# Kernel tuning notes

Hardware: AMD Instinct MI355X
Metric: run time of the kernel (lower is better)

The kernel has to match this reference:

```python
import jax, jax.numpy as jnp
import numpy as np

N_ELEMENTS = 64  # StructureElementLayer(n_elements=64)


def setup_inputs() -> dict:
    key = jax.random.key(0)
    k1, k2 = jax.random.split(key)
    # x: [N, C, T, V] skeleton sequence (batch, coord channels, time, joints)
    x = jax.random.normal(k1, (256, 3, 256, 25), dtype=jnp.float32)
    # StructureElementLayer parameters (torch.rand init / ones*3 init)
    centres = jax.random.uniform(k2, (N_ELEMENTS, 2), dtype=jnp.float32)
    sharpness = jnp.ones((N_ELEMENTS, 2), dtype=jnp.float32) * 3.0
    return {"x": x, "centres": centres, "sharpness": sharpness}


def _mst_deaths(D):
    """Dim-0 Vietoris-Rips persistence deaths == MST edge weights (Prim's algorithm).

    D: [n, n] symmetric distance matrix. Returns [n-1] finite death values
    (births are all 0; the single essential (0, inf) pair contributes
    exp(-inf)=0 to the structure-element layer and is dropped).
    """
    n = D.shape[0]
    in_tree = jnp.zeros((n,), dtype=bool).at[0].set(True)
    dist = D[0]  # min distance from each node to the current tree

    def step(carry, _):
        in_tree, dist = carry
        d = jnp.where(in_tree, jnp.inf, dist)
        j = jnp.argmin(d)
        w = d[j]
        in_tree = in_tree.at[j].set(True)
        dist = jnp.minimum(dist, D[j])
        return (in_tree, dist), w

    (_, _), deaths = jax.lax.scan(step, (in_tree, dist), None, length=n - 1)
    return deaths


def _forward(x, centres, sharpness):
    xm = x.mean(1)                                  # [N, T, V]
    diff = xm[..., :, None] - xm[..., None, :]      # [N, T, V, V] pairwise joint diffs
    diff = diff.mean(-3)                            # [N, V, V]
    feat = jnp.linalg.norm(diff, axis=1)            # [N, V]  (torch.norm(., 2, dim=1))
    feat = (feat - feat.min()) / (feat.max() - feat.min())
    # Euclidean distance matrix of the N points in V-dim space (grad-safe sqrt)
    sq = jnp.sum(feat * feat, axis=1)
    D2 = sq[:, None] + sq[None, :] - 2.0 * (feat @ feat.T)
    D2 = jnp.maximum(D2, 0.0)
    D = jnp.where(D2 > 0.0, jnp.sqrt(jnp.where(D2 > 0.0, D2, 1.0)), 0.0)
    deaths = _mst_deaths(D)                         # [N-1]
    diag = jnp.stack([jnp.zeros_like(deaths), deaths], axis=-1)  # [N-1, 2] (birth, death)
    # StructureElementLayer: sum_i exp(-sum_d (p_id - c_kd)^2 * s_kd^2)
    d2 = (diag[:, None, :] - centres[None, :, :]) ** 2            # [N-1, K, 2]
    out = jnp.exp(-(d2 * (sharpness ** 2)).sum(-1)).sum(0)        # [K]
    return out


def reference(x, centres, sharpness):
    return _forward(x, centres, sharpness)
```

## Files before the change

### kernel.cpp

```cpp
#include <hip/hip_runtime.h>
#include <hip/hip_fp16.h>


#define WS_M    0
#define WS_MM   25600
#define WS_RK   28672
#define WS_D16  65536

#define INF32 0xFFFFFFFFu

__global__ void k_mean(const float* __restrict__ x, float* __restrict__ m) {
    const int n = blockIdx.x;
    const int tid = threadIdx.x;
    __shared__ float sums[25];
    if (tid < 25) sums[tid] = 0.0f;
    __syncthreads();
    if (tid < 200) {
        const float* base = x + (long)n * 19200 + 4 * tid;
        float a0 = 0.f, a1 = 0.f, a2 = 0.f, a3 = 0.f;
        #pragma unroll
        for (int i = 0; i < 24; ++i) {
            float4 v = *reinterpret_cast<const float4*>(base + 800 * i);
            a0 += v.x; a1 += v.y; a2 += v.z; a3 += v.w;
        }
        const int v0 = (4 * tid) % 25;
        atomicAdd(&sums[v0], a0);
        atomicAdd(&sums[(v0 + 1) % 25], a1);
        atomicAdd(&sums[(v0 + 2) % 25], a2);
        atomicAdd(&sums[(v0 + 3) % 25], a3);
    }
    __syncthreads();
    if (tid < 25) m[n * 25 + tid] = sums[tid] * (1.0f / 768.0f);
}

template <int CTRL>
__device__ __forceinline__ unsigned int dpp_min_step(unsigned int v) {
    unsigned int t = (unsigned int)__builtin_amdgcn_update_dpp(
        (int)0xFFFFFFFF, (int)v, CTRL, 0xF, 0xF, false);
    return (t < v) ? t : v;
}

__global__ void __launch_bounds__(256) k_dist(const float* __restrict__ m,
                                              unsigned short* __restrict__ D16,
                                              unsigned int* __restrict__ rowKeyG,
                                              unsigned int* __restrict__ mm) {
    __shared__ float mS[6400];
    __shared__ float featS[6400];
    __shared__ unsigned int bmin, bmax;
    __shared__ unsigned int wred[4];
    const int i = blockIdx.x;
    const int t = threadIdx.x;
    if (t == 0) { bmin = 0x7F800000u; bmax = 0u; }
    #pragma unroll
    for (int it = 0; it < 7; ++it) {
        int o = it * 256 + t;
        if (o < 1600) reinterpret_cast<float4*>(mS)[o] =
            reinterpret_cast<const float4*>(m)[o];
    }
    __syncthreads();
    float r[25];
    #pragma unroll
    for (int v = 0; v < 25; ++v) r[v] = mS[t * 25 + v];
    float S1 = 0.f, S2 = 0.f;
    #pragma unroll
    for (int v = 0; v < 25; ++v) { S1 += r[v]; S2 += r[v] * r[v]; }
    float fmn = 1e30f, fmx = -1e30f;
    #pragma unroll
    for (int w = 0; w < 25; ++w) {
        float q = S2 - 2.f * r[w] * S1 + 25.f * r[w] * r[w];
        q = fmaxf(q, 0.f);
        float f = sqrtf(q);
        featS[t * 25 + w] = f;
        fmn = fminf(fmn, f); fmx = fmaxf(fmx, f);
    }
    if (i == 0) {
        atomicMin(&bmin, __float_as_uint(fmn));
        atomicMax(&bmax, __float_as_uint(fmx));
    }
    __syncthreads();
    if (i == 0 && t == 0) { mm[0] = bmin; mm[1] = bmax; }
    float fi[25];
    #pragma unroll
    for (int v = 0; v < 25; ++v) fi[v] = featS[i * 25 + v];
    float s = 0.f;
    #pragma unroll
    for (int v = 0; v < 25; ++v) { float d = fi[v] - featS[t * 25 + v]; s += d * d; }
    const unsigned int w16 = (unsigned int)__half_as_ushort(__float2half(s));
    D16[i * 256 + t] = (unsigned short)w16;
    const unsigned int lo = (i < t) ? i : t, hi = (i < t) ? t : i;
    unsigned int key = (t == i) ? INF32 : ((w16 << 16) | (lo << 8) | hi);
    key = dpp_min_step<0x111>(key);
    key = dpp_min_step<0x112>(key);
    key = dpp_min_step<0x114>(key);
    key = dpp_min_step<0x118>(key);
    key = dpp_min_step<0x142>(key);
    key = dpp_min_step<0x143>(key);
    if ((t & 63) == 63) wred[t >> 6] = key;
    __syncthreads();
    if (t == 0) {
        unsigned int b0 = wred[0] < wred[1] ? wred[0] : wred[1];
        unsigned int b1 = wred[2] < wred[3] ? wred[2] : wred[3];
        rowKeyG[i] = b0 < b1 ? b0 : b1;
    }
}

#define SA 132
#define SB 68
#define OFF_B (128 * SA)

__device__ __forceinline__ void wave0_phase(int n, int lane,
        unsigned int* rowKeyS, unsigned char* parentS, unsigned char* newidS,
        unsigned char* cmapS, float* deaths, unsigned int* ncS, unsigned int* dcS) {
    unsigned int par[4];
    #pragma unroll
    for (int s = 0; s < 4; ++s) {
        const int i = lane + 64 * s;
        if (i < n) {
            const unsigned int rk = rowKeyS[i];
            const unsigned int u = (rk >> 8) & 0xFFu, v = rk & 0xFFu;
            unsigned int p = (u == (unsigned int)i) ? v : u;
            if (rk == INF32) p = (unsigned int)i;
            par[s] = p;
            parentS[i] = (unsigned char)p;
        }
    }
    #pragma unroll
    for (int s = 0; s < 4; ++s) {
        const int i = lane + 64 * s;
        if (i < n) {
            const unsigned int p = par[s];
            if (p != (unsigned int)i) {
                const unsigned int mp = parentS[p];
                if (mp == (unsigned int)i && (unsigned int)i < p) {
                    parentS[i] = (unsigned char)i;
                } else {
                    const unsigned int d = atomicAdd(dcS, 1u);
                    const unsigned int rk = rowKeyS[i];
                    deaths[d] = sqrtf(__half2float(__ushort_as_half(
                        (unsigned short)(rk >> 16))));
                }
            }
        }
    }
    for (;;) {
        bool ch = false;
        #pragma unroll
        for (int s = 0; s < 4; ++s) {
            const int i = lane + 64 * s;
            if (i < n) {
                const unsigned char p0 = parentS[i];
                const unsigned char np = parentS[p0];
                if (np != p0) { ch = true; parentS[i] = np; }
            }
        }
        if (__ballot(ch) == 0ull) break;
    }
    #pragma unroll
    for (int s = 0; s < 4; ++s) {
        const int i = lane + 64 * s;
        if (i < n && parentS[i] == (unsigned char)i)
            newidS[i] = (unsigned char)atomicAdd(ncS, 1u);
    }
    #pragma unroll
    for (int s = 0; s < 4; ++s) {
        const int i = lane + 64 * s;
        if (i < n) cmapS[i] = newidS[parentS[i]];
    }
}

__global__ void __launch_bounds__(1024) k_mst(const unsigned short* __restrict__ D16g,
                                              const unsigned int* __restrict__ rowKeyG,
                                              const unsigned int* __restrict__ mm,
                                              const float* __restrict__ centres,
                                              const float* __restrict__ sharp,
                                              float* __restrict__ out) {
    __shared__ unsigned int Mb[128 * SA + 64 * SB];
    __shared__ unsigned int rowKeyS[256];
    __shared__ unsigned char parentS[256], newidS[256];
    __shared__ __align__(8) unsigned char cmapS[256];
    __shared__ unsigned int ncS, dcS;
    __shared__ float deaths[256];
    __shared__ float outpart[1024];
    const int tid = threadIdx.x;

    if (tid < 256) rowKeyS[tid] = rowKeyG[tid];
    if (tid == 0) { ncS = 0; dcS = 0; }
    __syncthreads();
    if (tid < 64)
        wave0_phase(256, tid, rowKeyS, parentS, newidS, cmapS, deaths, &ncS, &dcS);
    __syncthreads();
    int n = (int)ncS;

    if (n > 1) {
        for (int w = tid; w < n * SA; w += 1024) Mb[w] = INF32;
        __syncthreads();
        const int r = tid & 255, q = tid >> 8, jb0 = q * 64;
        const unsigned int cr = cmapS[r];
        const uint4* src = reinterpret_cast<const uint4*>(D16g) + r * 32 + q * 8;
        const uint2* cmv = reinterpret_cast<const uint2*>(cmapS);
        #pragma unroll
        for (int c8 = 0; c8 < 8; ++c8) {
            const uint4 w4 = src[c8];
            const uint2 c2 = cmv[q * 8 + c8];
            const unsigned int wds[4] = {w4.x, w4.y, w4.z, w4.w};
            const unsigned int cbs[2] = {c2.x, c2.y};
            #pragma unroll
            for (int u = 0; u < 8; ++u) {
                const unsigned int cj = (cbs[u >> 2] >> (8 * (u & 3))) & 0xFFu;
                if (cj != cr) {
                    const unsigned int w16 = (wds[u >> 1] >> (16 * (u & 1))) & 0xFFFFu;
                    const unsigned int lo = cr < cj ? cr : cj;
                    const unsigned int hi = cr < cj ? cj : cr;
                    atomicMin(&Mb[cr * SA + cj], (w16 << 16) | (lo << 8) | hi);
                }
            }
        }
        __syncthreads();
    }

    int srcOff = 0, srcStr = SA, dstOff = OFF_B, dstStr = SB;
    while (n > 1) {
        if (tid < n) rowKeyS[tid] = INF32;
        if (tid == 0) ncS = 0;
        __syncthreads();
        if (tid < 8 * n) {
            const int a = tid >> 3, sub = tid & 7;
            const unsigned int* row = &Mb[srcOff + a * srcStr];
            unsigned int best = INF32;
            for (int b = sub; b < n; b += 8) {
                const unsigned int v = row[b];
                best = v < best ? v : best;
            }
            if (best != INF32) atomicMin(&rowKeyS[a], best);
        }
        __syncthreads();
        if (tid < 64)
            wave0_phase(n, tid, rowKeyS, parentS, newidS, cmapS, deaths, &ncS, &dcS);
        __syncthreads();
        const int nc = (int)ncS;
        if (nc > 1) {
            for (int w = tid; w < nc * dstStr; w += 1024) Mb[dstOff + w] = INF32;
            __syncthreads();
            if (tid < 8 * n) {
                const int a = tid >> 3, sub = tid & 7;
                const unsigned int ca = cmapS[a];
                const unsigned int* row = &Mb[srcOff + a * srcStr];
                for (int b = sub; b < n; b += 8) {
                    const unsigned int cb = cmapS[b];
                    const unsigned int v = row[b];
                    if (ca != cb && v != INF32) {
                        const unsigned int lo = ca < cb ? ca : cb;
                        const unsigned int hi = ca < cb ? cb : ca;
                        atomicMin(&Mb[dstOff + ca * dstStr + cb],
                                  (v & 0xFFFF0000u) | (lo << 8) | hi);
                    }
                }
            }
            __syncthreads();
        }
        const int t1 = srcOff; srcOff = dstOff; dstOff = t1;
        const int t2 = srcStr; srcStr = dstStr; dstStr = t2;
        n = nc;
    }

    const float mn = __uint_as_float(mm[0]);
    const float mx = __uint_as_float(mm[1]);
    const float inv = 1.0f / (mx - mn);
    const int k = tid & 63;
    const int part = tid >> 6;
    const float c0 = centres[2 * k], c1 = centres[2 * k + 1];
    const float s0 = sharp[2 * k],   s1 = sharp[2 * k + 1];
    const float t0 = c0 * c0 * s0 * s0;
    const float s1sq = s1 * s1;
    float acc = 0.f;
    for (int idx = part; idx < 255; idx += 16) {
        const float d = deaths[idx] * inv - c1;
        acc += __expf(-(t0 + d * d * s1sq));
    }
    outpart[tid] = acc;
    __syncthreads();
    if (tid < 64) {
        float s = 0.f;
        #pragma unroll
        for (int pp = 0; pp < 16; ++pp) s += outpart[tid + 64 * pp];
        out[tid] = s;
    }
}

extern "C" void kernel_launch(void* const* d_in, const int* in_sizes, int n_in,
                              void* d_out, int out_size, void* d_ws, size_t ws_size,
                              hipStream_t stream) {
    const float* x       = (const float*)d_in[0];
    const float* centres = (const float*)d_in[1];
    const float* sharp   = (const float*)d_in[2];
    float* out = (float*)d_out;
    char* ws = (char*)d_ws;
    float*          m   = (float*)(ws + WS_M);
    unsigned int*   mm  = (unsigned int*)(ws + WS_MM);
    unsigned int*   rk  = (unsigned int*)(ws + WS_RK);
    unsigned short* D16 = (unsigned short*)(ws + WS_D16);

    k_mean<<<256, 256, 0, stream>>>(x, m);
    k_dist<<<256, 256, 0, stream>>>(m, D16, rk, mm);
    k_mst<<<1, 1024, 0, stream>>>(D16, rk, mm, centres, sharp, out);
}
```

Baseline: 96.03 us.

## Offload first Boruvka contraction to a parallel multi-block kernel

Adds a new k_contract kernel with 256 blocks. Each block recomputes the first component labelling and scatters its row of the 16-bit distance matrix into a global contracted matrix with global atomicMin. The single-block k_mst then only copies that matrix into LDS instead of running 65536 atomic updates itself. The contracted matrix is initialised inside k_mean. Component renumbering now uses a wave ballot/popcount prefix instead of atomicAdd, and the round loop is capped at 12. The trade-off is an extra kernel launch, global atomics and redundant labelling work in every block.

```diff
diff --git a/kernel.cpp b/kernel.cpp
--- a/kernel.cpp
+++ b/kernel.cpp
@@ -6,12 +6,16 @@
 #define WS_MM   25600
 #define WS_RK   28672
 #define WS_D16  65536
+#define WS_MP   196608
 
 #define INF32 0xFFFFFFFFu
-
-__global__ void k_mean(const float* __restrict__ x, float* __restrict__ m) {
+#define MPSTR 132
+
+__global__ void k_mean(const float* __restrict__ x, float* __restrict__ m,
+                       unsigned int* __restrict__ Mp) {
     const int n = blockIdx.x;
     const int tid = threadIdx.x;
+    if (tid < 66) Mp[n * 66 + tid] = INF32;
     __shared__ float sums[25];
     if (tid < 25) sums[tid] = 0.0f;
     __syncthreads();
@@ -104,10 +108,7 @@
     }
 }
 
-#define SA 132
-#define SB 68
-#define OFF_B (128 * SA)
-
+template <bool RECORD>
 __device__ __forceinline__ void wave0_phase(int n, int lane,
         unsigned int* rowKeyS, unsigned char* parentS, unsigned char* newidS,
         unsigned char* cmapS, float* deaths, unsigned int* ncS, unsigned int* dcS) {
@@ -130,10 +131,9 @@
         if (i < n) {
             const unsigned int p = par[s];
             if (p != (unsigned int)i) {
-                const unsigned int mp = parentS[p];
-                if (mp == (unsigned int)i && (unsigned int)i < p) {
+                if (parentS[p] == (unsigned char)i && (unsigned int)i < p) {
                     parentS[i] = (unsigned char)i;
-                } else {
+                } else if (RECORD) {
                     const unsigned int d = atomicAdd(dcS, 1u);
                     const unsigned int rk = rowKeyS[i];
                     deaths[d] = sqrtf(__half2float(__ushort_as_half(
@@ -155,12 +155,24 @@
         }
         if (__ballot(ch) == 0ull) break;
     }
+    bool isr[4];
     #pragma unroll
     for (int s = 0; s < 4; ++s) {
         const int i = lane + 64 * s;
-        if (i < n && parentS[i] == (unsigned char)i)
-            newidS[i] = (unsigned char)atomicAdd(ncS, 1u);
-    }
+        isr[s] = (i < n) && (parentS[i] == (unsigned char)i);
+    }
+    unsigned int base = 0;
+    const unsigned long long below = (1ull << lane) - 1ull;
+    #pragma unroll
+    for (int s = 0; s < 4; ++s) {
+        const unsigned long long mask = __ballot(isr[s]);
+        if (isr[s]) {
+            const int i = lane + 64 * s;
+            newidS[i] = (unsigned char)(base + __popcll(mask & below));
+        }
+        base += (unsigned int)__popcll(mask);
+    }
+    if (lane == 0) *ncS = base;
     #pragma unroll
     for (int s = 0; s < 4; ++s) {
         const int i = lane + 64 * s;
@@ -168,7 +180,35 @@
     }
 }
 
-__global__ void __launch_bounds__(1024) k_mst(const unsigned short* __restrict__ D16g,
+__global__ void __launch_bounds__(256) k_contract(const unsigned short* __restrict__ D16g,
+                                                  const unsigned int* __restrict__ rowKeyG,
+                                                  unsigned int* __restrict__ Mp) {
+    __shared__ unsigned int rowKeyS[256];
+    __shared__ unsigned char parentS[256], newidS[256], cmapS[256];
+    __shared__ unsigned int ncS;
+    const int tid = threadIdx.x;
+    const int b = blockIdx.x;
+    rowKeyS[tid] = rowKeyG[tid];
+    __syncthreads();
+    if (tid < 64)
+        wave0_phase<false>(256, tid, rowKeyS, parentS, newidS, cmapS,
+                           nullptr, &ncS, nullptr);
+    __syncthreads();
+    const unsigned int ca = cmapS[b];
+    const unsigned int cb = cmapS[tid];
+    if (ca != cb) {
+        const unsigned int w16 = (unsigned int)D16g[b * 256 + tid];
+        const unsigned int lo = ca < cb ? ca : cb;
+        const unsigned int hi = ca < cb ? cb : ca;
+        atomicMin(&Mp[ca * MPSTR + cb], (w16 << 16) | (lo << 8) | hi);
+    }
+}
+
+#define SA 132
+#define SB 68
+#define OFF_B (128 * SA)
+
+__global__ void __launch_bounds__(1024) k_mst(const unsigned int* __restrict__ Mp,
                                               const unsigned int* __restrict__ rowKeyG,
                                               const unsigned int* __restrict__ mm,
                                               const float* __restrict__ centres,
@@ -176,66 +216,42 @@
                                               float* __restrict__ out) {
     __shared__ unsigned int Mb[128 * SA + 64 * SB];
     __shared__ unsigned int rowKeyS[256];
-    __shared__ unsigned char parentS[256], newidS[256];
-    __shared__ __align__(8) unsigned char cmapS[256];
+    __shared__ unsigned char parentS[256], newidS[256], cmapS[256];
     __shared__ unsigned int ncS, dcS;
     __shared__ float deaths[256];
     __shared__ float outpart[1024];
     const int tid = threadIdx.x;
 
     if (tid < 256) rowKeyS[tid] = rowKeyG[tid];
-    if (tid == 0) { ncS = 0; dcS = 0; }
+    if (tid == 0) dcS = 0;
     __syncthreads();
     if (tid < 64)
-        wave0_phase(256, tid, rowKeyS, parentS, newidS, cmapS, deaths, &ncS, &dcS);
+        wave0_phase<true>(256, tid, rowKeyS, parentS, newidS, cmapS,
+                          deaths, &ncS, &dcS);
     __syncthreads();
     int n = (int)ncS;
 
-    if (n > 1) {
-        for (int w = tid; w < n * SA; w += 1024) Mb[w] = INF32;
-        __syncthreads();
-        const int r = tid & 255, q = tid >> 8, jb0 = q * 64;
-        const unsigned int cr = cmapS[r];
-        const uint4* src = reinterpret_cast<const uint4*>(D16g) + r * 32 + q * 8;
-        const uint2* cmv = reinterpret_cast<const uint2*>(cmapS);
-        #pragma unroll
-        for (int c8 = 0; c8 < 8; ++c8) {
-            const uint4 w4 = src[c8];
-            const uint2 c2 = cmv[q * 8 + c8];
-            const unsigned int wds[4] = {w4.x, w4.y, w4.z, w4.w};
-            const unsigned int cbs[2] = {c2.x, c2.y};
-            #pragma unroll
-            for (int u = 0; u < 8; ++u) {
-                const unsigned int cj = (cbs[u >> 2] >> (8 * (u & 3))) & 0xFFu;
-                if (cj != cr) {
-                    const unsigned int w16 = (wds[u >> 1] >> (16 * (u & 1))) & 0xFFFFu;
-                    const unsigned int lo = cr < cj ? cr : cj;
-                    const unsigned int hi = cr < cj ? cj : cr;
-                    atomicMin(&Mb[cr * SA + cj], (w16 << 16) | (lo << 8) | hi);
-                }
-            }
-        }
-        __syncthreads();
-    }
+    for (int idx = tid; idx < n * SA; idx += 1024) Mb[idx] = Mp[idx];
+    __syncthreads();
 
     int srcOff = 0, srcStr = SA, dstOff = OFF_B, dstStr = SB;
-    while (n > 1) {
+    for (int round = 0; round < 12 && n > 1; ++round) {
         if (tid < n) rowKeyS[tid] = INF32;
-        if (tid == 0) ncS = 0;
         __syncthreads();
         if (tid < 8 * n) {
             const int a = tid >> 3, sub = tid & 7;
             const unsigned int* row = &Mb[srcOff + a * srcStr];
             unsigned int best = INF32;
-            for (int b = sub; b < n; b += 8) {
-                const unsigned int v = row[b];
+            for (int b2 = sub; b2 < n; b2 += 8) {
+                const unsigned int v = row[b2];
                 best = v < best ? v : best;
             }
             if (best != INF32) atomicMin(&rowKeyS[a], best);
         }
         __syncthreads();
         if (tid < 64)
-            wave0_phase(n, tid, rowKeyS, parentS, newidS, cmapS, deaths, &ncS, &dcS);
+            wave0_phase<true>(n, tid, rowKeyS, parentS, newidS, cmapS,
+                              deaths, &ncS, &dcS);
         __syncthreads();
         const int nc = (int)ncS;
         if (nc > 1) {
@@ -245,9 +261,9 @@
                 const int a = tid >> 3, sub = tid & 7;
                 const unsigned int ca = cmapS[a];
                 const unsigned int* row = &Mb[srcOff + a * srcStr];
-                for (int b = sub; b < n; b += 8) {
-                    const unsigned int cb = cmapS[b];
-                    const unsigned int v = row[b];
+                for (int b2 = sub; b2 < n; b2 += 8) {
+                    const unsigned int cb = cmapS[b2];
+                    const unsigned int v = row[b2];
                     if (ca != cb && v != INF32) {
                         const unsigned int lo = ca < cb ? ca : cb;
                         const unsigned int hi = ca < cb ? cb : ca;
@@ -299,8 +315,10 @@
     unsigned int*   mm  = (unsigned int*)(ws + WS_MM);
     unsigned int*   rk  = (unsigned int*)(ws + WS_RK);
     unsigned short* D16 = (unsigned short*)(ws + WS_D16);
-
-    k_mean<<<256, 256, 0, stream>>>(x, m);
+    unsigned int*   Mp  = (unsigned int*)(ws + WS_MP);
+
+    k_mean<<<256, 256, 0, stream>>>(x, m, Mp);
     k_dist<<<256, 256, 0, stream>>>(m, D16, rk, mm);
-    k_mst<<<1, 1024, 0, stream>>>(D16, rk, mm, centres, sharp, out);
-}
+    k_contract<<<256, 256, 0, stream>>>(D16, rk, Mp);
+    k_mst<<<1, 1024, 0, stream>>>(Mp, rk, mm, centres, sharp, out);
+}
```

Result: faster. 93.64 us (-2.5%).
